# Optimization experiments

Measured on AMD Instinct MI355X. Metric: run time of the kernel, lower is better.

Reference implementation:

```python
import jax, jax.numpy as jnp
import numpy as np

SEQ_LEN = 2048
EMBED = 1024
HIDDEN = 1024
BATCH = 8

def setup_inputs() -> dict:
    key = jax.random.key(0)
    ks = jax.random.split(key, 7)
    scale = (6.0 / (EMBED + HIDDEN)) ** 0.5  # xavier_uniform
    inputs = jax.random.normal(ks[0], (BATCH, SEQ_LEN, EMBED), dtype=jnp.float32)
    Wq = jax.random.uniform(ks[1], (EMBED, HIDDEN), minval=-scale, maxval=scale, dtype=jnp.float32)
    Wk = jax.random.uniform(ks[2], (EMBED, HIDDEN), minval=-scale, maxval=scale, dtype=jnp.float32)
    Wv = jax.random.uniform(ks[3], (EMBED, HIDDEN), minval=-scale, maxval=scale, dtype=jnp.float32)
    bq = jax.random.normal(ks[4], (HIDDEN,), dtype=jnp.float32) * 0.01
    bk = jax.random.normal(ks[5], (HIDDEN,), dtype=jnp.float32) * 0.01
    bv = jax.random.normal(ks[6], (HIDDEN,), dtype=jnp.float32) * 0.01
    return {"inputs": inputs, "Wq": Wq, "bq": bq, "Wk": Wk, "bk": bk, "Wv": Wv, "bv": bv}

def reference(inputs, Wq, bq, Wk, bk, Wv, bv):
    # inputs: [B, S, E]
    q = jnp.einsum('bse,eh->bsh', inputs, Wq) + bq  # [B,S,H]
    k = jnp.einsum('bse,eh->bsh', inputs, Wk) + bk
    v = jnp.einsum('bse,eh->bsh', inputs, Wv) + bv
    scores = jnp.einsum('bqh,bkh->bqk', q, k) / jnp.sqrt(jnp.float32(HIDDEN))  # [B,S,S]
    causal = jnp.tril(jnp.ones((SEQ_LEN, SEQ_LEN), dtype=bool))
    scores = jnp.where(causal, scores, -jnp.inf)
    attn = jax.nn.softmax(scores, axis=-1)
    return jnp.einsum('bqk,bkh->bqh', attn, v)
```

## Files before the change

### kernel.cpp

```cpp
#include <hip/hip_runtime.h>

#define B_ 8
#define S_ 2048
#define E_ 1024
#define H_ 1024

typedef __attribute__((ext_vector_type(8))) short bf16x8;
typedef __attribute__((ext_vector_type(4))) float f32x4;

__device__ inline short f2bf(float f) {
  unsigned u = __builtin_bit_cast(unsigned, f);
  unsigned r = u + 0x7FFFu + ((u >> 16) & 1u);
  return (short)(r >> 16);
}
__device__ inline float bf2f(short s) {
  unsigned u = ((unsigned)(unsigned short)s) << 16;
  return __builtin_bit_cast(float, u);
}

__device__ inline void async16(const void* g, void* l) {
  __builtin_amdgcn_global_load_lds((const __attribute__((address_space(1))) void*)g,
                                   (__attribute__((address_space(3))) void*)l,
                                   16, 0, 0);
}

__global__ __launch_bounds__(256)
void prep(const float* __restrict__ X, short* __restrict__ Xbf,
          const float* __restrict__ W0, const float* __restrict__ W1,
          const float* __restrict__ W2, short* __restrict__ Wt) {
  __shared__ __align__(16) float t[64][65];
  const int bid = blockIdx.x;
  if (bid < 2048) {
    const int n4 = (int)((size_t)B_ * S_ * E_ / 4);
    const int stride = 2048 * 256;
    for (int i = bid * 256 + threadIdx.x; i < n4; i += stride) {
      float4 v = ((const float4*)X)[i];
      short4 o;
      o.x = f2bf(v.x); o.y = f2bf(v.y); o.z = f2bf(v.z); o.w = f2bf(v.w);
      ((short4*)Xbf)[i] = o;
    }
    return;
  }
  const int idx = bid - 2048;
  const int zz = idx >> 8;
  const int rem = idx & 255;
  const float* W = (zz == 0) ? W0 : (zz == 1) ? W1 : W2;
  short* out = Wt + (size_t)zz * H_ * E_;
  const int h0 = (rem & 15) * 64, e0 = (rem >> 4) * 64;
  const int r = threadIdx.x >> 4;
  const int c = (threadIdx.x & 15) * 4;
#pragma unroll
  for (int p = 0; p < 4; ++p) {
    int rr = r + p * 16;
    float4 v = *(const float4*)&W[(size_t)(e0 + rr) * H_ + h0 + c];
    t[rr][c + 0] = v.x; t[rr][c + 1] = v.y; t[rr][c + 2] = v.z; t[rr][c + 3] = v.w;
  }
  __syncthreads();
#pragma unroll
  for (int p = 0; p < 4; ++p) {
    int rr = r + p * 16;
    short4 o;
    o.x = f2bf(t[c + 0][rr]); o.y = f2bf(t[c + 1][rr]);
    o.z = f2bf(t[c + 2][rr]); o.w = f2bf(t[c + 3][rr]);
    *(short4*)&out[(size_t)(h0 + rr) * E_ + e0 + c] = o;
  }
}

#define BAR() asm volatile("s_barrier" ::: "memory")
#define VMC(n) asm volatile("s_waitcnt vmcnt(" #n ")" ::: "memory")

#define RD_B(buf, ks)                                                        \
  _Pragma("unroll")                                                          \
  for (int n = 0; n < 4; ++n)                                                \
    bfr[n] = *(const bf16x8*)(lBp + (buf) * 32768 + (ks) * 16384 +           \
                              ((wc * 64 + n * 16 + lr) << 6) + aCol)

#define RD_A(buf, ks, mh)                                                    \
  _Pragma("unroll")                                                          \
  for (int m = 0; m < 4; ++m)                                                \
    af[m] = *(const bf16x8*)(lAp + (buf) * 32768 + (ks) * 16384 +            \
                             ((wr * 128 + (mh) * 64 + m * 16 + lr) << 6) + aCol)

#define MFMA16(mh)                                                           \
  _Pragma("unroll")                                                          \
  for (int m = 0; m < 4; ++m) {                                              \
    _Pragma("unroll")                                                        \
    for (int n = 0; n < 4; ++n)                                              \
      acc[(mh) * 4 + m][n] = __builtin_amdgcn_mfma_f32_16x16x32_bf16(        \
          af[m], bfr[n], acc[(mh) * 4 + m][n], 0, 0, 0);                     \
  }

#define STAGE_A(buf, ks, kt) do {                                            \
    const short* _s = A + (size_t)(m0 + srow) * ldA + (kt) * 64 + (ks) * 32 + scol; \
    char* _d = (char*)lAp + (buf) * 32768 + (ks) * 16384 + wv * 1024;        \
    async16(_s, _d);                                                         \
    async16(_s + (size_t)128 * ldA, _d + 8192);                              \
  } while (0)

#define STAGE_B(buf, ks, kt) do {                                            \
    const short* _s = Bt + (size_t)(n0 + srow) * ldBt + (kt) * 64 + (ks) * 32 + scol; \
    char* _d = (char*)lBp + (buf) * 32768 + (ks) * 16384 + wv * 1024;        \
    async16(_s, _d);                                                         \
    async16(_s + (size_t)128 * ldBt, _d + 8192);                             \
  } while (0)

#define PHASE(buf, ks, mh, STG, WT) do {                                     \
    if ((mh) == 0) { RD_B(buf, ks); }                                        \
    RD_A(buf, ks, mh);                                                       \
    STG;                                                                     \
    WT;                                                                      \
    BAR();                                                                   \
    asm volatile("s_waitcnt lgkmcnt(0)" ::: "memory");                       \
    __builtin_amdgcn_sched_barrier(0);                                       \
    __builtin_amdgcn_s_setprio(1);                                           \
    MFMA16(mh);                                                              \
    __builtin_amdgcn_s_setprio(0);                                           \
    BAR();                                                                   \
  } while (0)

template <int MODE>
__global__ __launch_bounds__(512, 2)
void gemm8(const short* __restrict__ A, const short* __restrict__ Bt,
           void* __restrict__ C0, void* __restrict__ C1, void* __restrict__ C2,
           const float* __restrict__ b0, const float* __restrict__ b1,
           const float* __restrict__ b2,
           int K, int ldA, int ldBt, int ldC, float scale) {
  int bx, by;
  {
    const int bid = blockIdx.x;
    int t = (bid & 7) * 96 + (bid >> 3);
    by = t / 12; bx = t % 12;
  }

  __shared__ __align__(16) short lA[2][2][256 * 32];
  __shared__ __align__(16) short lB[2][2][256 * 32];
  const char* lAp = (const char*)&lA[0][0][0];
  const char* lBp = (const char*)&lB[0][0][0];

  const int tid = threadIdx.x;
  const int lane = tid & 63;
  const int wv = tid >> 6;
  const int wr = wv >> 2, wc = wv & 3;
  const int lr = lane & 15, kg = lane >> 4;
  const int m0 = by * 256, n0 = bx * 256;
  const int nt = K >> 6;
  const int nIter = nt >> 1;

  const int aCol = (kg * 16) ^ ((lr & 8) << 2);
  const int srow = tid >> 2;
  const int scol = (((tid & 3) * 16) ^ (tid & 32)) >> 1;

  f32x4 acc[8][4];
#pragma unroll
  for (int m = 0; m < 8; ++m)
#pragma unroll
    for (int n = 0; n < 4; ++n) acc[m][n] = (f32x4){0.f, 0.f, 0.f, 0.f};
  bf16x8 bfr[4], af[4];

  STAGE_B(0, 0, 0); STAGE_A(0, 0, 0); STAGE_B(0, 1, 0); STAGE_A(0, 1, 0);
  STAGE_B(1, 0, 1); STAGE_A(1, 0, 1); STAGE_B(1, 1, 1);
  VMC(6);
  BAR();

  for (int i = 0; i < nIter; ++i) {
    const int T = 2 * i;
    const bool lastI = (i == nIter - 1);
    PHASE(0, 0, 0, STAGE_A(1, 1, T + 1), (void)0);
    PHASE(0, 0, 1, if (!lastI) { STAGE_B(0, 0, T + 2); }, (void)0);
    PHASE(0, 1, 0, if (!lastI) { STAGE_A(0, 0, T + 2); }, (void)0);
    PHASE(0, 1, 1, if (!lastI) { STAGE_B(0, 1, T + 2); },
          if (lastI) { VMC(0); } else { VMC(6); });
    PHASE(1, 0, 0, if (!lastI) { STAGE_A(0, 1, T + 2); }, (void)0);
    PHASE(1, 0, 1, if (!lastI) { STAGE_B(1, 0, T + 3); }, (void)0);
    PHASE(1, 1, 0, if (!lastI) { STAGE_A(1, 0, T + 3); }, (void)0);
    PHASE(1, 1, 1, if (!lastI) { STAGE_B(1, 1, T + 3); },
          if (!lastI) { VMC(6); });
  }

  if ((n0 >> 10) == 2) {
    short* tv = (short*)lAp;
    const int zb = by >> 3;
    const int sb = (by & 7) * 256;
    short* VT = (short*)C2 + (size_t)zb * H_ * S_;
    const int hseg = n0 - 2048;
#pragma unroll
    for (int p = 0; p < 2; ++p) {
      if ((wc >> 1) == p) {
#pragma unroll
        for (int mq = 0; mq < 8; ++mq) {
          int sr = wr * 128 + (mq >> 2) * 64 + (mq & 3) * 16 + kg * 4;
#pragma unroll
          for (int n = 0; n < 4; ++n) {
            int c = wc * 64 + n * 16 + lr;
            float bb = b2[hseg + c];
            f32x4 v = acc[mq][n];
            short4 o;
            o.x = f2bf(v[0] + bb); o.y = f2bf(v[1] + bb);
            o.z = f2bf(v[2] + bb); o.w = f2bf(v[3] + bb);
            *(short4*)&tv[(c & 127) * 264 + sr] = o;
          }
        }
      }
      __syncthreads();
#pragma unroll
      for (int i = 0; i < 8; ++i) {
        int chunk = i * 512 + tid;
        int h = chunk >> 5, sc = (chunk & 31) * 8;
        bf16x8 v8 = *(const bf16x8*)&tv[h * 264 + sc];
        *(bf16x8*)&VT[(size_t)(hseg + p * 128 + h) * S_ + sb + sc] = v8;
      }
      __syncthreads();
    }
    return;
  }
#pragma unroll
  for (int mq = 0; mq < 8; ++mq) {
    int rowb = m0 + wr * 128 + (mq >> 2) * 64 + (mq & 3) * 16 + kg * 4;
#pragma unroll
    for (int n = 0; n < 4; ++n) {
      int col = n0 + wc * 64 + n * 16 + lr;
      f32x4 v = acc[mq][n];
      int seg = n0 >> 10;
      const float* bp = (seg == 0) ? b0 : b1;
      short* C = (short*)((seg == 0) ? C0 : C1);
      int cl = col & 1023;
      float bb = bp[cl];
#pragma unroll
      for (int r = 0; r < 4; ++r)
        C[(size_t)(rowb + r) * ldC + cl] = f2bf(v[r] + bb);
    }
  }
}


#define RD_B4(ks)                                                            \
  _Pragma("unroll")                                                          \
  for (int n = 0; n < 4; ++n)                                                \
    bfr[n] = *(const bf16x8*)(lBp + (ks) * 16384 +                           \
                              ((wc * 64 + n * 16 + lr) << 6) + aCol)

#define RD_A4(ks)                                                            \
  _Pragma("unroll")                                                          \
  for (int m = 0; m < 4; ++m)                                                \
    af[m] = *(const bf16x8*)(lAp + (ks) * 8192 +                             \
                             ((wr * 64 + m * 16 + lr) << 6) + aCol)

#define MFMA16Q()                                                            \
  _Pragma("unroll")                                                          \
  for (int m = 0; m < 4; ++m) {                                              \
    _Pragma("unroll")                                                        \
    for (int n = 0; n < 4; ++n)                                              \
      acc[m][n] = __builtin_amdgcn_mfma_f32_16x16x32_bf16(                   \
          af[m], bfr[n], acc[m][n], 0, 0, 0);                                \
  }

template <int MODE>
__global__ __launch_bounds__(512, 4)
void gemm4(const short* __restrict__ A, const short* __restrict__ Bt,
           void* __restrict__ C0, float* __restrict__ PlO,
           int K, int ldA, int ldBt, int ldC,
           size_t zsA, size_t zsB, size_t zsC, float scale) {
  const int z = blockIdx.x & 7;
  const int rr0 = blockIdx.x >> 3;
  int bx, by;
  if (MODE == 1) {
    by = 0; int ac = 0;
    while (rr0 >= ac + (by >> 1) + 1) { ac += (by >> 1) + 1; ++by; }
    bx = rr0 - ac;
  } else {
    by = 15 - (rr0 >> 2); bx = rr0 & 3;
  }
  A  += (size_t)z * zsA;
  Bt += (size_t)z * zsB;

  __shared__ __align__(16) short lA[2][128 * 32];
  __shared__ __align__(16) short lB[2][256 * 32];
  __shared__ float sLi[128];
  const char* lAp = (const char*)&lA[0][0];
  const char* lBp = (const char*)&lB[0][0];

  const int tid = threadIdx.x;
  const int lane = tid & 63;
  const int wv = tid >> 6;
  const int wr = wv >> 2, wc = wv & 3;
  const int lr = lane & 15, kg = lane >> 4;
  const int m0 = by * 128, n0 = bx * 256;
  const int kEnd = (MODE == 2) ? ((by >> 1) + 1) * 256 : K;
  const int nt = kEnd >> 6;

  const int aCol = (kg * 16) ^ ((lr & 8) << 2);
  const int srow = tid >> 2;
  const int scol = (((tid & 3) * 16) ^ (tid & 32)) >> 1;

  if (MODE == 2 && tid < 128) {
    float l = 0.f;
    for (int kt = 0; kt <= (by >> 1); ++kt)
      l += PlO[((size_t)z * 8 + kt) * S_ + m0 + tid];
    sLi[tid] = 1.f / l;
  }

  f32x4 acc[4][4];
#pragma unroll
  for (int m = 0; m < 4; ++m)
#pragma unroll
    for (int n = 0; n < 4; ++n) acc[m][n] = (f32x4){0.f, 0.f, 0.f, 0.f};
  bf16x8 bfr[4], af[4];

  for (int t = 0; t < nt; ++t) {
    {
      const short* sA = A + (size_t)(m0 + srow) * ldA + t * 64 + scol;
      const short* sB = Bt + (size_t)(n0 + srow) * ldBt + t * 64 + scol;
      char* dA = (char*)lAp + tid * 16;
      char* dB = (char*)lBp + tid * 16;
      async16(sA, dA);
      async16(sA + 32, dA + 8192);
      async16(sB, dB);
      async16(sB + (size_t)128 * ldBt, dB + 8192);
      async16(sB + 32, dB + 16384);
      async16(sB + (size_t)128 * ldBt + 32, dB + 24576);
    }
    VMC(0);
    BAR();
    RD_B4(0); RD_A4(0);
    asm volatile("s_waitcnt lgkmcnt(0)" ::: "memory");
    __builtin_amdgcn_sched_barrier(0);
    __builtin_amdgcn_s_setprio(1);
    MFMA16Q();
    __builtin_amdgcn_s_setprio(0);
    RD_B4(1); RD_A4(1);
    asm volatile("s_waitcnt lgkmcnt(0)" ::: "memory");
    __builtin_amdgcn_sched_barrier(0);
    __builtin_amdgcn_s_setprio(1);
    MFMA16Q();
    __builtin_amdgcn_s_setprio(0);
    BAR();
  }

  if (MODE == 1) {
    float* tmpL = (float*)lAp;
    short* C = (short*)C0 + (size_t)z * zsC;
    const bool diag = (bx == (by >> 1));
#pragma unroll
    for (int m = 0; m < 4; ++m) {
      int rt0 = wr * 64 + m * 16 + kg * 4;
#pragma unroll
      for (int r = 0; r < 4; ++r) {
        int rt = rt0 + r;
        float se = 0.f;
#pragma unroll
        for (int n = 0; n < 4; ++n) {
          int c = wc * 64 + n * 16 + lr;
          bool ok = !diag || (n0 + c <= m0 + rt);
          short sh = ok ? f2bf(__expf(acc[m][n][r] * scale)) : (short)0;
          se += bf2f(sh);
          C[(size_t)(m0 + rt) * ldC + n0 + c] = sh;
        }
#pragma unroll
        for (int o = 1; o < 16; o <<= 1) se += __shfl_xor(se, o);
        if (lr == 0) tmpL[rt * 4 + wc] = se;
      }
    }
    __syncthreads();
    if (tid < 128) {
      float l = tmpL[tid * 4 + 0] + tmpL[tid * 4 + 1] +
                tmpL[tid * 4 + 2] + tmpL[tid * 4 + 3];
      PlO[((size_t)z * 8 + bx) * S_ + m0 + tid] = l;
    }
    return;
  }
  {
    float* C = (float*)C0 + (size_t)z * zsC;
#pragma unroll
    for (int m = 0; m < 4; ++m) {
      int rl = wr * 64 + m * 16 + kg * 4;
      f32x4 liv = *(const f32x4*)&sLi[rl];
      int rowb = m0 + rl;
#pragma unroll
      for (int n = 0; n < 4; ++n) {
        int col = n0 + wc * 64 + n * 16 + lr;
        f32x4 v = acc[m][n];
#pragma unroll
        for (int r = 0; r < 4; ++r)
          C[(size_t)(rowb + r) * ldC + col] = v[r] * liv[r];
      }
    }
  }
}

extern "C" void kernel_launch(void* const* d_in, const int* in_sizes, int n_in,
                              void* d_out, int out_size, void* d_ws, size_t ws_size,
                              hipStream_t stream) {
  const float* X  = (const float*)d_in[0];
  const float* Wq = (const float*)d_in[1];
  const float* bq = (const float*)d_in[2];
  const float* Wk = (const float*)d_in[3];
  const float* bk = (const float*)d_in[4];
  const float* Wv = (const float*)d_in[5];
  const float* bv = (const float*)d_in[6];

  char* ws = (char*)d_ws;
  const size_t MB = 1024ull * 1024ull;
  short* Pbuf = (short*)ws;
  short* Xbf  = (short*)ws;
  short* Q    = (short*)(ws + 64 * MB);
  short* Kb   = (short*)(ws + 96 * MB);
  short* Vt   = (short*)(ws + 128 * MB);
  short* Wt   = (short*)(ws + 160 * MB);
  float* Pl   = (float*)(ws + 160 * MB);

  prep<<<2816, 256, 0, stream>>>(X, Xbf, Wq, Wk, Wv, Wt);
  gemm8<0><<<768, 512, 0, stream>>>(
      Xbf, Wt, Q, Kb, Vt, bq, bk, bv, E_, E_, E_, H_, 1.f);
  gemm4<1><<<576, 512, 0, stream>>>(
      Q, Kb, Pbuf, Pl, H_, H_, H_, S_,
      (size_t)S_ * H_, (size_t)S_ * H_, (size_t)S_ * S_, 0.03125f);
  gemm4<2><<<512, 512, 0, stream>>>(
      Pbuf, Vt, d_out, Pl, S_, S_, S_, H_,
      (size_t)S_ * S_, (size_t)H_ * S_, (size_t)S_ * H_, 1.f);
}
```

Before: 254.3 us.

## Use 128x128 causal tiles for scores and finer K bounds in PV

Replaces the templated score GEMM with a dedicated 128x128-tile kernel on 256 threads, enumerating only lower-triangular tiles to avoid computing masked upper blocks. The PV kernel now bounds its K loop at 128-column granularity and reorders row blocks to interleave long and short rows. Row sums are stored as 16 partials per row instead of 8. Smaller score tiles reduce per-block data reuse and add more blocks.

Result: faster. 245.3 us (-3.5%).

```diff
diff --git a/kernel.cpp b/kernel.cpp
--- a/kernel.cpp
+++ b/kernel.cpp
@@ -118,13 +118,12 @@
     BAR();                                                                   \
   } while (0)
 
-template <int MODE>
 __global__ __launch_bounds__(512, 2)
 void gemm8(const short* __restrict__ A, const short* __restrict__ Bt,
            void* __restrict__ C0, void* __restrict__ C1, void* __restrict__ C2,
            const float* __restrict__ b0, const float* __restrict__ b1,
            const float* __restrict__ b2,
-           int K, int ldA, int ldBt, int ldC, float scale) {
+           int K, int ldA, int ldBt, int ldC) {
   int bx, by;
   {
     const int bid = blockIdx.x;
@@ -233,18 +232,6 @@
 }
 
 
-#define RD_B4(ks)                                                            \
-  _Pragma("unroll")                                                          \
-  for (int n = 0; n < 4; ++n)                                                \
-    bfr[n] = *(const bf16x8*)(lBp + (ks) * 16384 +                           \
-                              ((wc * 64 + n * 16 + lr) << 6) + aCol)
-
-#define RD_A4(ks)                                                            \
-  _Pragma("unroll")                                                          \
-  for (int m = 0; m < 4; ++m)                                                \
-    af[m] = *(const bf16x8*)(lAp + (ks) * 8192 +                             \
-                             ((wr * 64 + m * 16 + lr) << 6) + aCol)
-
 #define MFMA16Q()                                                            \
   _Pragma("unroll")                                                          \
   for (int m = 0; m < 4; ++m) {                                              \
@@ -254,24 +241,113 @@
           af[m], bfr[n], acc[m][n], 0, 0, 0);                                \
   }
 
-template <int MODE>
+__global__ __launch_bounds__(256, 4)
+void sc128(const short* __restrict__ Q, const short* __restrict__ Kb,
+           short* __restrict__ P, float* __restrict__ Pl, float scale) {
+  const int z = blockIdx.x & 7;
+  int rr0 = blockIdx.x >> 3;
+  int by = 0, ac = 0;
+  while (rr0 >= ac + by + 1) { ac += by + 1; ++by; }
+  const int bx = rr0 - ac;
+  const short* A  = Q  + (size_t)z * S_ * H_;
+  const short* Bt = Kb + (size_t)z * S_ * H_;
+
+  __shared__ __align__(16) short lA[2][128 * 32];
+  __shared__ __align__(16) short lB[2][128 * 32];
+  const char* lAp = (const char*)&lA[0][0];
+  const char* lBp = (const char*)&lB[0][0];
+
+  const int tid = threadIdx.x;
+  const int lane = tid & 63;
+  const int wv = tid >> 6;
+  const int wr = wv >> 1, wc = wv & 1;
+  const int lr = lane & 15, kg = lane >> 4;
+  const int m0 = by * 128, n0 = bx * 128;
+
+  const int aCol = (kg * 16) ^ ((lr & 8) << 2);
+  const int srow = tid >> 2;
+  const int scol = (((tid & 3) * 16) ^ (tid & 32)) >> 1;
+
+  f32x4 acc[4][4];
+#pragma unroll
+  for (int m = 0; m < 4; ++m)
+#pragma unroll
+    for (int n = 0; n < 4; ++n) acc[m][n] = (f32x4){0.f, 0.f, 0.f, 0.f};
+  bf16x8 bfr[4], af[4];
+
+  for (int t = 0; t < 16; ++t) {
+    const short* sA = A  + (size_t)(m0 + srow) * H_ + t * 64 + scol;
+    const short* sB = Bt + (size_t)(n0 + srow) * H_ + t * 64 + scol;
+#pragma unroll
+    for (int ks = 0; ks < 2; ++ks) {
+      char* dA = (char*)lAp + ks * 8192 + tid * 16;
+      char* dB = (char*)lBp + ks * 8192 + tid * 16;
+      async16(sA + ks * 32, dA);
+      async16(sA + ks * 32 + (size_t)64 * H_, dA + 4096);
+      async16(sB + ks * 32, dB);
+      async16(sB + ks * 32 + (size_t)64 * H_, dB + 4096);
+    }
+    VMC(0);
+    BAR();
+#pragma unroll
+    for (int ks = 0; ks < 2; ++ks) {
+#pragma unroll
+      for (int n = 0; n < 4; ++n)
+        bfr[n] = *(const bf16x8*)(lBp + ks * 8192 +
+                                  ((wc * 64 + n * 16 + lr) << 6) + aCol);
+#pragma unroll
+      for (int m = 0; m < 4; ++m)
+        af[m] = *(const bf16x8*)(lAp + ks * 8192 +
+                                 ((wr * 64 + m * 16 + lr) << 6) + aCol);
+      asm volatile("s_waitcnt lgkmcnt(0)" ::: "memory");
+      __builtin_amdgcn_sched_barrier(0);
+      __builtin_amdgcn_s_setprio(1);
+      MFMA16Q();
+      __builtin_amdgcn_s_setprio(0);
+    }
+    BAR();
+  }
+
+  float* tmpL = (float*)lAp;
+  short* C = P + (size_t)z * S_ * S_;
+  const bool diag = (bx == by);
+#pragma unroll
+  for (int m = 0; m < 4; ++m) {
+    int rt0 = wr * 64 + m * 16 + kg * 4;
+#pragma unroll
+    for (int r = 0; r < 4; ++r) {
+      int rt = rt0 + r;
+      float se = 0.f;
+#pragma unroll
+      for (int n = 0; n < 4; ++n) {
+        int c = wc * 64 + n * 16 + lr;
+        bool ok = !diag || (c <= rt);
+        short sh = ok ? f2bf(__expf(acc[m][n][r] * scale)) : (short)0;
+        se += bf2f(sh);
+        C[(size_t)(m0 + rt) * S_ + n0 + c] = sh;
+      }
+#pragma unroll
+      for (int o = 1; o < 16; o <<= 1) se += __shfl_xor(se, o);
+      if (lr == 0) tmpL[rt * 2 + wc] = se;
+    }
+  }
+  __syncthreads();
+  if (tid < 128) {
+    float l = tmpL[tid * 2 + 0] + tmpL[tid * 2 + 1];
+    Pl[((size_t)z * 16 + bx) * S_ + m0 + tid] = l;
+  }
+}
+
 __global__ __launch_bounds__(512, 4)
-void gemm4(const short* __restrict__ A, const short* __restrict__ Bt,
-           void* __restrict__ C0, float* __restrict__ PlO,
-           int K, int ldA, int ldBt, int ldC,
-           size_t zsA, size_t zsB, size_t zsC, float scale) {
+void pv128(const short* __restrict__ A, const short* __restrict__ Bt,
+           float* __restrict__ C0, const float* __restrict__ Pl) {
   const int z = blockIdx.x & 7;
   const int rr0 = blockIdx.x >> 3;
-  int bx, by;
-  if (MODE == 1) {
-    by = 0; int ac = 0;
-    while (rr0 >= ac + (by >> 1) + 1) { ac += (by >> 1) + 1; ++by; }
-    bx = rr0 - ac;
-  } else {
-    by = 15 - (rr0 >> 2); bx = rr0 & 3;
-  }
-  A  += (size_t)z * zsA;
-  Bt += (size_t)z * zsB;
+  const int j = rr0 >> 2;
+  const int by = (j < 8) ? (15 - j) : (j - 8);
+  const int bx = rr0 & 3;
+  const short* Ap  = A  + (size_t)z * S_ * S_;
+  const short* Btp = Bt + (size_t)z * H_ * S_;
 
   __shared__ __align__(16) short lA[2][128 * 32];
   __shared__ __align__(16) short lB[2][256 * 32];
@@ -285,17 +361,16 @@
   const int wr = wv >> 2, wc = wv & 3;
   const int lr = lane & 15, kg = lane >> 4;
   const int m0 = by * 128, n0 = bx * 256;
-  const int kEnd = (MODE == 2) ? ((by >> 1) + 1) * 256 : K;
-  const int nt = kEnd >> 6;
+  const int nt = (by + 1) * 2;
 
   const int aCol = (kg * 16) ^ ((lr & 8) << 2);
   const int srow = tid >> 2;
   const int scol = (((tid & 3) * 16) ^ (tid & 32)) >> 1;
 
-  if (MODE == 2 && tid < 128) {
+  if (tid < 128) {
     float l = 0.f;
-    for (int kt = 0; kt <= (by >> 1); ++kt)
-      l += PlO[((size_t)z * 8 + kt) * S_ + m0 + tid];
+    for (int kt = 0; kt <= by; ++kt)
+      l += Pl[((size_t)z * 16 + kt) * S_ + m0 + tid];
     sLi[tid] = 1.f / l;
   }
 
@@ -308,81 +383,51 @@
 
   for (int t = 0; t < nt; ++t) {
     {
-      const short* sA = A + (size_t)(m0 + srow) * ldA + t * 64 + scol;
-      const short* sB = Bt + (size_t)(n0 + srow) * ldBt + t * 64 + scol;
+      const short* sA = Ap  + (size_t)(m0 + srow) * S_ + t * 64 + scol;
+      const short* sB = Btp + (size_t)(n0 + srow) * S_ + t * 64 + scol;
       char* dA = (char*)lAp + tid * 16;
       char* dB = (char*)lBp + tid * 16;
       async16(sA, dA);
       async16(sA + 32, dA + 8192);
       async16(sB, dB);
-      async16(sB + (size_t)128 * ldBt, dB + 8192);
+      async16(sB + (size_t)128 * S_, dB + 8192);
       async16(sB + 32, dB + 16384);
-      async16(sB + (size_t)128 * ldBt + 32, dB + 24576);
+      async16(sB + (size_t)128 * S_ + 32, dB + 24576);
     }
     VMC(0);
     BAR();
-    RD_B4(0); RD_A4(0);
-    asm volatile("s_waitcnt lgkmcnt(0)" ::: "memory");
-    __builtin_amdgcn_sched_barrier(0);
-    __builtin_amdgcn_s_setprio(1);
-    MFMA16Q();
-    __builtin_amdgcn_s_setprio(0);
-    RD_B4(1); RD_A4(1);
-    asm volatile("s_waitcnt lgkmcnt(0)" ::: "memory");
-    __builtin_amdgcn_sched_barrier(0);
-    __builtin_amdgcn_s_setprio(1);
-    MFMA16Q();
-    __builtin_amdgcn_s_setprio(0);
+#pragma unroll
+    for (int ks = 0; ks < 2; ++ks) {
+#pragma unroll
+      for (int n = 0; n < 4; ++n)
+        bfr[n] = *(const bf16x8*)(lBp + ks * 16384 +
+                                  ((wc * 64 + n * 16 + lr) << 6) + aCol);
+#pragma unroll
+      for (int m = 0; m < 4; ++m)
+        af[m] = *(const bf16x8*)(lAp + ks * 8192 +
+                                 ((wr * 64 + m * 16 + lr) << 6) + aCol);
+      asm volatile("s_waitcnt lgkmcnt(0)" ::: "memory");
+      __builtin_amdgcn_sched_barrier(0);
+      __builtin_amdgcn_s_setprio(1);
+      MFMA16Q();
+      __builtin_amdgcn_s_setprio(0);
+    }
     BAR();
   }
 
-  if (MODE == 1) {
-    float* tmpL = (float*)lAp;
-    short* C = (short*)C0 + (size_t)z * zsC;
-    const bool diag = (bx == (by >> 1));
-#pragma unroll
-    for (int m = 0; m < 4; ++m) {
-      int rt0 = wr * 64 + m * 16 + kg * 4;
-#pragma unroll
-      for (int r = 0; r < 4; ++r) {
-        int rt = rt0 + r;
-        float se = 0.f;
-#pragma unroll
-        for (int n = 0; n < 4; ++n) {
-          int c = wc * 64 + n * 16 + lr;
-          bool ok = !diag || (n0 + c <= m0 + rt);
-          short sh = ok ? f2bf(__expf(acc[m][n][r] * scale)) : (short)0;
-          se += bf2f(sh);
-          C[(size_t)(m0 + rt) * ldC + n0 + c] = sh;
-        }
-#pragma unroll
-        for (int o = 1; o < 16; o <<= 1) se += __shfl_xor(se, o);
-        if (lr == 0) tmpL[rt * 4 + wc] = se;
-      }
-    }
-    __syncthreads();
-    if (tid < 128) {
-      float l = tmpL[tid * 4 + 0] + tmpL[tid * 4 + 1] +
-                tmpL[tid * 4 + 2] + tmpL[tid * 4 + 3];
-      PlO[((size_t)z * 8 + bx) * S_ + m0 + tid] = l;
-    }
-    return;
-  }
-  {
-    float* C = (float*)C0 + (size_t)z * zsC;
-#pragma unroll
-    for (int m = 0; m < 4; ++m) {
-      int rl = wr * 64 + m * 16 + kg * 4;
-      f32x4 liv = *(const f32x4*)&sLi[rl];
-      int rowb = m0 + rl;
-#pragma unroll
-      for (int n = 0; n < 4; ++n) {
-        int col = n0 + wc * 64 + n * 16 + lr;
-        f32x4 v = acc[m][n];
-#pragma unroll
-        for (int r = 0; r < 4; ++r)
-          C[(size_t)(rowb + r) * ldC + col] = v[r] * liv[r];
-      }
+  float* C = C0 + (size_t)z * S_ * H_;
+#pragma unroll
+  for (int m = 0; m < 4; ++m) {
+    int rl = wr * 64 + m * 16 + kg * 4;
+    f32x4 liv = *(const f32x4*)&sLi[rl];
+    int rowb = m0 + rl;
+#pragma unroll
+    for (int n = 0; n < 4; ++n) {
+      int col = n0 + wc * 64 + n * 16 + lr;
+      f32x4 v = acc[m][n];
+#pragma unroll
+      for (int r = 0; r < 4; ++r)
+        C[(size_t)(rowb + r) * H_ + col] = v[r] * liv[r];
     }
   }
 }
@@ -409,12 +454,8 @@
   float* Pl   = (float*)(ws + 160 * MB);
 
   prep<<<2816, 256, 0, stream>>>(X, Xbf, Wq, Wk, Wv, Wt);
-  gemm8<0><<<768, 512, 0, stream>>>(
-      Xbf, Wt, Q, Kb, Vt, bq, bk, bv, E_, E_, E_, H_, 1.f);
-  gemm4<1><<<576, 512, 0, stream>>>(
-      Q, Kb, Pbuf, Pl, H_, H_, H_, S_,
-      (size_t)S_ * H_, (size_t)S_ * H_, (size_t)S_ * S_, 0.03125f);
-  gemm4<2><<<512, 512, 0, stream>>>(
-      Pbuf, Vt, d_out, Pl, S_, S_, S_, H_,
-      (size_t)S_ * S_, (size_t)H_ * S_, (size_t)S_ * H_, 1.f);
-}
+  gemm8<<<768, 512, 0, stream>>>(
+      Xbf, Wt, Q, Kb, Vt, bq, bk, bv, E_, E_, E_, H_);
+  sc128<<<1088, 256, 0, stream>>>(Q, Kb, Pbuf, Pl, 0.03125f);
+  pv128<<<512, 512, 0, stream>>>(Pbuf, Vt, (float*)d_out, Pl);
+}
```
